# Kernel tuning notes

Hardware: AMD Instinct MI355X
Metric: run time of the kernel (lower is better)

The kernel has to match this reference:

```python
import jax, jax.numpy as jnp
import numpy as np

DECAY = 0.999
EPS = 1e-06
NUM_CLUSTERS = 512
NUM_HEADS = 8
DIM_PER_HEAD = 64


def setup_inputs() -> dict:
    key = jax.random.key(0)
    k1, k2 = jax.random.split(key)
    x = jax.random.normal(k1, (8, 2048, NUM_HEADS * DIM_PER_HEAD), dtype=jnp.float32)
    means = jax.random.normal(k2, (NUM_HEADS, NUM_CLUSTERS, DIM_PER_HEAD), dtype=jnp.float32)
    return {"x": x, "means": means}


def reference(x, means):
    b, n, _ = x.shape
    h, k, d = means.shape
    xh = x.reshape(b, n, h, d)  # 'b n (h d) -> b n h d'
    dists = (
        jnp.sum(xh ** 2, axis=-1)[..., None]
        - 2.0 * jnp.einsum('bnhd,hkd->bnhk', xh, means)
        + jnp.sum(means ** 2, axis=-1)[None, None, :, :]
    )
    cluster_ids = jnp.argmin(dists, axis=-1)  # [b, n, h] int
    # training-path EMA codebook update
    one_hot = jax.nn.one_hot(cluster_ids, k, dtype=jnp.float32)  # [b, n, h, k]
    per_cluster_count = jnp.sum(one_hot, axis=(0, 1))  # [h, k]
    sum_x = jnp.einsum('bnhk,bnhd->hkd', one_hot, xh)  # [h, k, d]
    new_means = sum_x / (EPS + per_cluster_count[..., None])
    updated_means = (1.0 - DECAY) * new_means + DECAY * means
    return cluster_ids, updated_means
```

## Files before the change

### kernel.cpp

```cpp
#include <hip/hip_runtime.h>

#define NUM_HEADS 8
#define DIM 64
#define NCLUST 512
#define NTOK 16384
#define ROWLEN 512
#define NIDS (NTOK * NUM_HEADS)
#define NMEANS (NUM_HEADS * NCLUST * DIM)
#define NCK (NUM_HEADS * NCLUST)
#define TPB 128
#define KQ 128
#define CAP 8
#define DELTA 0.35f

typedef unsigned long long u64;
typedef short bf16x8 __attribute__((ext_vector_type(8)));
typedef float f32x4 __attribute__((ext_vector_type(4)));

__device__ __forceinline__ unsigned short f2bf(float f) {
    unsigned b = __float_as_uint(f);
    return (unsigned short)((b + 0x7fffu + ((b >> 16) & 1u)) >> 16);
}
__device__ __forceinline__ unsigned pack2bf(float lo, float hi) {
    return (unsigned)f2bf(lo) | ((unsigned)f2bf(hi) << 16);
}
__device__ __forceinline__ float bf2f(unsigned short b) {
    return __uint_as_float((unsigned)b << 16);
}
__device__ __forceinline__ u64 packkey(float s, int k) {
    unsigned u = __float_as_uint(s);
    unsigned ord = (u & 0x80000000u) ? ~u : (u | 0x80000000u);
    return ((u64)(~ord) << 32) | (unsigned)k;
}
__device__ __forceinline__ int swz(int row, int byte_in_row) {
    return row * 128 + (byte_in_row ^ ((row & 7) << 4));
}

__global__ void vq_prep(const float* __restrict__ means,
                        float* __restrict__ q,
                        unsigned short* __restrict__ mbf) {
    int g = blockIdx.x * blockDim.x + threadIdx.x;
    int row = g >> 4, c = g & 15;
    float4 v = *(const float4*)(means + (size_t)row * DIM + c * 4);
    ushort4 b;
    b.x = f2bf(v.x); b.y = f2bf(v.y); b.z = f2bf(v.z); b.w = f2bf(v.w);
    *(ushort4*)(mbf + (size_t)row * DIM + c * 4) = b;
    float s = fmaf(v.x, v.x, fmaf(v.y, v.y, fmaf(v.z, v.z, v.w * v.w)));
#pragma unroll
    for (int off = 1; off < 16; off <<= 1) s += __shfl_xor(s, off, 64);
    if (c == 0) q[row] = 0.5f * s;
}

__global__ __launch_bounds__(256, 4) void vq_score(const float* __restrict__ x,
                                                   const float* __restrict__ means,
                                                   const unsigned short* __restrict__ mbf,
                                                   const float* __restrict__ q,
                                                   float* __restrict__ ids_f) {
    __shared__ __align__(16) unsigned char msq[KQ * 128];
    __shared__ __align__(16) unsigned char xbb[TPB * 128];
    __shared__ float qs[NCLUST];
    __shared__ int cnt[TPB];
    __shared__ unsigned short candL[TPB][CAP];

    const int head = blockIdx.y;
    const int t0   = blockIdx.x * TPB;
    const int tid  = threadIdx.x;
    const int wv = tid >> 6, l = tid & 63;
    const int lg = l >> 4, lc = l & 15;
    const int twave = wv * 32;

    uint4 pf0, pf1, pf2, pf3;
    auto loadq = [&](int qt) {
        int row = tid >> 1, c = tid & 1;
        const uint4* src = (const uint4*)(mbf +
            ((size_t)head * NCLUST + qt * KQ + row) * DIM + c * 32);
        pf0 = src[0]; pf1 = src[1]; pf2 = src[2]; pf3 = src[3];
    };
    auto writems = [&]() {
        int row = tid >> 1, c = tid & 1;
        *(uint4*)(msq + swz(row, c * 64 + 0))  = pf0;
        *(uint4*)(msq + swz(row, c * 64 + 16)) = pf1;
        *(uint4*)(msq + swz(row, c * 64 + 32)) = pf2;
        *(uint4*)(msq + swz(row, c * 64 + 48)) = pf3;
    };

#pragma unroll
    for (int it = 0; it < 2; ++it) {
        int tok = (tid >> 2) + it * 64;
        int c = tid & 3;
        const float4* src = (const float4*)(x + (size_t)(t0 + tok) * ROWLEN + head * DIM + c * 16);
        float4 v0 = src[0], v1 = src[1], v2 = src[2], v3 = src[3];
        uint4 lo, hi;
        lo.x = pack2bf(v0.x, v0.y); lo.y = pack2bf(v0.z, v0.w);
        lo.z = pack2bf(v1.x, v1.y); lo.w = pack2bf(v1.z, v1.w);
        hi.x = pack2bf(v2.x, v2.y); hi.y = pack2bf(v2.z, v2.w);
        hi.z = pack2bf(v3.x, v3.y); hi.w = pack2bf(v3.z, v3.w);
        *(uint4*)(xbb + swz(tok, c * 32 + 0))  = lo;
        *(uint4*)(xbb + swz(tok, c * 32 + 16)) = hi;
    }
    qs[tid] = q[head * NCLUST + tid];
    qs[tid + 256] = q[head * NCLUST + tid + 256];
    if (tid < TPB) cnt[tid] = 0;
    loadq(0);
    __syncthreads();

    bf16x8 af[2][2];
#pragma unroll
    for (int tt = 0; tt < 2; ++tt)
#pragma unroll
        for (int ks = 0; ks < 2; ++ks)
            af[tt][ks] = *(const bf16x8*)(xbb + swz(twave + tt * 16 + lc, ks * 64 + lg * 16));

    float best[2][4];
#pragma unroll
    for (int tt = 0; tt < 2; ++tt)
#pragma unroll
        for (int r = 0; r < 4; ++r) best[tt][r] = -3.0e38f;
    float thr[2][4];

    auto sweep1_q = [&](int qt) {
        const int rbase = 511 - qt * KQ - lc;
#pragma unroll
        for (int ct = 0; ct < KQ / 16; ++ct) {
            bf16x8 b0 = *(const bf16x8*)(msq + swz(ct * 16 + lc, 0 + lg * 16));
            bf16x8 b1 = *(const bf16x8*)(msq + swz(ct * 16 + lc, 64 + lg * 16));
            float qv = qs[qt * KQ + ct * 16 + lc];
            int rk = rbase - ct * 16;
#pragma unroll
            for (int tt = 0; tt < 2; ++tt) {
                f32x4 acc = (f32x4){-qv, -qv, -qv, -qv};
                acc = __builtin_amdgcn_mfma_f32_16x16x32_bf16(af[tt][0], b0, acc, 0, 0, 0);
                acc = __builtin_amdgcn_mfma_f32_16x16x32_bf16(af[tt][1], b1, acc, 0, 0, 0);
#pragma unroll
                for (int r = 0; r < 4; ++r) {
                    float v = __uint_as_float((__float_as_uint(acc[r]) & 0xFFFFFE00u) | (unsigned)rk);
                    best[tt][r] = fmaxf(best[tt][r], v);
                }
            }
        }
    };
    auto collect_q = [&](int qt) {
#pragma unroll
        for (int ct = 0; ct < KQ / 16; ++ct) {
            bf16x8 b0 = *(const bf16x8*)(msq + swz(ct * 16 + lc, 0 + lg * 16));
            bf16x8 b1 = *(const bf16x8*)(msq + swz(ct * 16 + lc, 64 + lg * 16));
            float qv = qs[qt * KQ + ct * 16 + lc];
            int k = qt * KQ + ct * 16 + lc;
#pragma unroll
            for (int tt = 0; tt < 2; ++tt) {
                f32x4 acc = (f32x4){-qv, -qv, -qv, -qv};
                acc = __builtin_amdgcn_mfma_f32_16x16x32_bf16(af[tt][0], b0, acc, 0, 0, 0);
                acc = __builtin_amdgcn_mfma_f32_16x16x32_bf16(af[tt][1], b1, acc, 0, 0, 0);
#pragma unroll
                for (int r = 0; r < 4; ++r) {
                    if (acc[r] >= thr[tt][r]) {
                        int tok = twave + tt * 16 + lg * 4 + r;
                        int slot = atomicAdd(&cnt[tok], 1);
                        if (slot < CAP) candL[tok][slot] = (unsigned short)k;
                    }
                }
            }
        }
    };

    for (int qt = 0; qt < 4; ++qt) {
        __syncthreads();
        writems();
        if (qt < 3) loadq(qt + 1);
        __syncthreads();
        sweep1_q(qt);
    }
#pragma unroll
    for (int tt = 0; tt < 2; ++tt)
#pragma unroll
        for (int r = 0; r < 4; ++r) {
#pragma unroll
            for (int off = 1; off < 16; off <<= 1)
                best[tt][r] = fmaxf(best[tt][r], __shfl_xor(best[tt][r], off, 64));
            thr[tt][r] = best[tt][r] - DELTA;
        }

    loadq(2);
    collect_q(3);
    for (int qt = 2; qt >= 0; --qt) {
        __syncthreads();
        writems();
        if (qt > 0) loadq(qt - 1);
        __syncthreads();
        collect_q(qt);
    }
    __syncthreads();

#pragma unroll 2
    for (int g = 0; g < 8; ++g) {
        int tok = twave + g * 4 + lg;
        int n = cnt[tok]; n = n < CAP ? n : CAP;
        const float4 xv = *(const float4*)(x + (size_t)(t0 + tok) * ROWLEN + head * DIM + lc * 4);
        u64 bk = ~0ull;
        for (int j = 0; j < n; ++j) {
            int k = candL[tok][j];
            const float4 mv = *(const float4*)(means + ((size_t)head * NCLUST + k) * DIM + lc * 4);
            float p = fmaf(xv.x, mv.x, fmaf(xv.y, mv.y, fmaf(xv.z, mv.z, xv.w * mv.w)));
#pragma unroll
            for (int off = 1; off < 16; off <<= 1) p += __shfl_xor(p, off, 64);
            u64 cd = packkey(p - qs[k], k);
            bk = cd < bk ? cd : bk;
        }
        if (lc == 0) ids_f[(size_t)(t0 + tok) * NUM_HEADS + head] = (float)(unsigned)(bk & 0x1ffu);
    }
}

__global__ void vq_scatter(const float* __restrict__ x,
                           const float* __restrict__ ids_f,
                           float* __restrict__ counts,
                           unsigned short* __restrict__ sums_bf,
                           int rep_mask) {
    int g = blockIdx.x * blockDim.x + threadIdx.x;
    int p = g >> 5;
    int l32 = threadIdx.x & 31;
    int token = p >> 3;
    int h = p & 7;
    int rep = token & rep_mask;
    int id = (int)ids_f[p];
    float2 xv = *(const float2*)(x + (size_t)token * ROWLEN + h * DIM + l32 * 2);
    unsigned val = pack2bf(xv.x, xv.y);
    unsigned short* dst = sums_bf + (size_t)rep * NMEANS
                        + (((size_t)h * NCLUST + id) << 6) + l32 * 2;
    asm volatile("global_atomic_pk_add_bf16 %0, %1, off" :: "v"(dst), "v"(val) : "memory");
    if (l32 == 0) atomicAdd(&counts[rep * NCK + h * NCLUST + id], 1.0f);
}

__global__ void vq_final(const float* __restrict__ means,
                         const float* __restrict__ counts,
                         const unsigned short* __restrict__ sums_bf,
                         float* __restrict__ out_means,
                         int nrep) {
    int i = blockIdx.x * blockDim.x + threadIdx.x;
    int ck = i >> 6;
    float c = 0.f, s = 0.f;
    for (int r = 0; r < nrep; ++r) {
        c += counts[r * NCK + ck];
        s += bf2f(sums_bf[(size_t)r * NMEANS + i]);
    }
    float nm = s / (1e-6f + c);
    out_means[i] = 0.999f * means[i] + 0.001f * nm;
}

extern "C" void kernel_launch(void* const* d_in, const int* in_sizes, int n_in,
                              void* d_out, int out_size, void* d_ws, size_t ws_size,
                              hipStream_t stream) {
    const float* x     = (const float*)d_in[0];
    const float* means = (const float*)d_in[1];

    float* out       = (float*)d_out;
    float* ids_f     = out;
    float* out_means = out + NIDS;

    float*          q   = (float*)d_ws;
    unsigned short* mbf = (unsigned short*)(q + NCK);
    float*          fbase = (float*)(mbf + NMEANS);
    size_t core = (size_t)((char*)fbase - (char*)d_ws);

    size_t per_rep = (size_t)NCK * sizeof(float) + (size_t)NMEANS * sizeof(unsigned short);
    int nrep = 1;
    for (int r = 8; r > 1; r >>= 1) {
        if (ws_size >= core + (size_t)r * per_rep) { nrep = r; break; }
    }
    float*          counts  = fbase;
    unsigned short* sums_bf = (unsigned short*)(counts + (size_t)nrep * NCK);

    hipMemsetAsync(counts, 0, (size_t)nrep * per_rep, stream);

    vq_prep<<<(NCK * 16) / 256, 256, 0, stream>>>(means, q, mbf);

    dim3 gs(NTOK / TPB, NUM_HEADS);
    vq_score<<<gs, 256, 0, stream>>>(x, means, mbf, q, ids_f);

    vq_scatter<<<(NIDS * 32) / 256, 256, 0, stream>>>(x, ids_f, counts, sums_bf, nrep - 1);

    vq_final<<<NMEANS / 256, 256, 0, stream>>>(means, counts, sums_bf, out_means, nrep);
}
```

Before: 78.14 us.

## Halve tokens per block, load x fragments directly into registers

Tokens per block drop from 128 to 64, so each wave handles 16 tokens instead of 32. The x staging buffer in shared memory is removed, and each lane now loads its MFMA A-fragment straight from global memory and converts it to bf16. Launch bounds rise to 8 blocks per CU to allow more occupancy thanks to fewer registers and less LDS. In exchange, the grid doubles, so the codebook tiles are streamed through shared memory twice as often per token, and there is less MFMA reuse per B-fragment load.

```diff
diff --git a/kernel.cpp b/kernel.cpp
--- a/kernel.cpp
+++ b/kernel.cpp
@@ -8,7 +8,7 @@
 #define NIDS (NTOK * NUM_HEADS)
 #define NMEANS (NUM_HEADS * NCLUST * DIM)
 #define NCK (NUM_HEADS * NCLUST)
-#define TPB 128
+#define TPB 64
 #define KQ 128
 #define CAP 8
 #define DELTA 0.35f
@@ -51,13 +51,12 @@
     if (c == 0) q[row] = 0.5f * s;
 }
 
-__global__ __launch_bounds__(256, 4) void vq_score(const float* __restrict__ x,
+__global__ __launch_bounds__(256, 8) void vq_score(const float* __restrict__ x,
                                                    const float* __restrict__ means,
                                                    const unsigned short* __restrict__ mbf,
                                                    const float* __restrict__ q,
                                                    float* __restrict__ ids_f) {
     __shared__ __align__(16) unsigned char msq[KQ * 128];
-    __shared__ __align__(16) unsigned char xbb[TPB * 128];
     __shared__ float qs[NCLUST];
     __shared__ int cnt[TPB];
     __shared__ unsigned short candL[TPB][CAP];
@@ -67,7 +66,7 @@
     const int tid  = threadIdx.x;
     const int wv = tid >> 6, l = tid & 63;
     const int lg = l >> 4, lc = l & 15;
-    const int twave = wv * 32;
+    const int twave = wv * 16;
 
     uint4 pf0, pf1, pf2, pf3;
     auto loadq = [&](int qt) {
@@ -84,39 +83,27 @@
         *(uint4*)(msq + swz(row, c * 64 + 48)) = pf3;
     };
 
-#pragma unroll
-    for (int it = 0; it < 2; ++it) {
-        int tok = (tid >> 2) + it * 64;
-        int c = tid & 3;
-        const float4* src = (const float4*)(x + (size_t)(t0 + tok) * ROWLEN + head * DIM + c * 16);
-        float4 v0 = src[0], v1 = src[1], v2 = src[2], v3 = src[3];
-        uint4 lo, hi;
-        lo.x = pack2bf(v0.x, v0.y); lo.y = pack2bf(v0.z, v0.w);
-        lo.z = pack2bf(v1.x, v1.y); lo.w = pack2bf(v1.z, v1.w);
-        hi.x = pack2bf(v2.x, v2.y); hi.y = pack2bf(v2.z, v2.w);
-        hi.z = pack2bf(v3.x, v3.y); hi.w = pack2bf(v3.z, v3.w);
-        *(uint4*)(xbb + swz(tok, c * 32 + 0))  = lo;
-        *(uint4*)(xbb + swz(tok, c * 32 + 16)) = hi;
+    bf16x8 af[2];
+    {
+        const float* xrow = x + (size_t)(t0 + twave + lc) * ROWLEN + head * DIM;
+#pragma unroll
+        for (int ks = 0; ks < 2; ++ks) {
+            float av[8];
+            *(float4*)&av[0] = *(const float4*)(xrow + ks * 32 + lg * 8);
+            *(float4*)&av[4] = *(const float4*)(xrow + ks * 32 + lg * 8 + 4);
+#pragma unroll
+            for (int j = 0; j < 8; ++j) af[ks][j] = (short)f2bf(av[j]);
+        }
     }
     qs[tid] = q[head * NCLUST + tid];
     qs[tid + 256] = q[head * NCLUST + tid + 256];
     if (tid < TPB) cnt[tid] = 0;
     loadq(0);
-    __syncthreads();
-
-    bf16x8 af[2][2];
-#pragma unroll
-    for (int tt = 0; tt < 2; ++tt)
-#pragma unroll
-        for (int ks = 0; ks < 2; ++ks)
-            af[tt][ks] = *(const bf16x8*)(xbb + swz(twave + tt * 16 + lc, ks * 64 + lg * 16));
-
-    float best[2][4];
-#pragma unroll
-    for (int tt = 0; tt < 2; ++tt)
-#pragma unroll
-        for (int r = 0; r < 4; ++r) best[tt][r] = -3.0e38f;
-    float thr[2][4];
+
+    float best[4];
+#pragma unroll
+    for (int r = 0; r < 4; ++r) best[r] = -3.0e38f;
+    float thr[4];
 
     auto sweep1_q = [&](int qt) {
         const int rbase = 511 - qt * KQ - lc;
@@ -126,16 +113,13 @@
             bf16x8 b1 = *(const bf16x8*)(msq + swz(ct * 16 + lc, 64 + lg * 16));
             float qv = qs[qt * KQ + ct * 16 + lc];
             int rk = rbase - ct * 16;
-#pragma unroll
-            for (int tt = 0; tt < 2; ++tt) {
-                f32x4 acc = (f32x4){-qv, -qv, -qv, -qv};
-                acc = __builtin_amdgcn_mfma_f32_16x16x32_bf16(af[tt][0], b0, acc, 0, 0, 0);
-                acc = __builtin_amdgcn_mfma_f32_16x16x32_bf16(af[tt][1], b1, acc, 0, 0, 0);
-#pragma unroll
-                for (int r = 0; r < 4; ++r) {
-                    float v = __uint_as_float((__float_as_uint(acc[r]) & 0xFFFFFE00u) | (unsigned)rk);
-                    best[tt][r] = fmaxf(best[tt][r], v);
-                }
+            f32x4 acc = (f32x4){-qv, -qv, -qv, -qv};
+            acc = __builtin_amdgcn_mfma_f32_16x16x32_bf16(af[0], b0, acc, 0, 0, 0);
+            acc = __builtin_amdgcn_mfma_f32_16x16x32_bf16(af[1], b1, acc, 0, 0, 0);
+#pragma unroll
+            for (int r = 0; r < 4; ++r) {
+                float v = __uint_as_float((__float_as_uint(acc[r]) & 0xFFFFFE00u) | (unsigned)rk);
+                best[r] = fmaxf(best[r], v);
             }
         }
     };
@@ -146,18 +130,15 @@
             bf16x8 b1 = *(const bf16x8*)(msq + swz(ct * 16 + lc, 64 + lg * 16));
             float qv = qs[qt * KQ + ct * 16 + lc];
             int k = qt * KQ + ct * 16 + lc;
-#pragma unroll
-            for (int tt = 0; tt < 2; ++tt) {
-                f32x4 acc = (f32x4){-qv, -qv, -qv, -qv};
-                acc = __builtin_amdgcn_mfma_f32_16x16x32_bf16(af[tt][0], b0, acc, 0, 0, 0);
-                acc = __builtin_amdgcn_mfma_f32_16x16x32_bf16(af[tt][1], b1, acc, 0, 0, 0);
-#pragma unroll
-                for (int r = 0; r < 4; ++r) {
-                    if (acc[r] >= thr[tt][r]) {
-                        int tok = twave + tt * 16 + lg * 4 + r;
-                        int slot = atomicAdd(&cnt[tok], 1);
-                        if (slot < CAP) candL[tok][slot] = (unsigned short)k;
-                    }
+            f32x4 acc = (f32x4){-qv, -qv, -qv, -qv};
+            acc = __builtin_amdgcn_mfma_f32_16x16x32_bf16(af[0], b0, acc, 0, 0, 0);
+            acc = __builtin_amdgcn_mfma_f32_16x16x32_bf16(af[1], b1, acc, 0, 0, 0);
+#pragma unroll
+            for (int r = 0; r < 4; ++r) {
+                if (acc[r] >= thr[r]) {
+                    int tok = twave + lg * 4 + r;
+                    int slot = atomicAdd(&cnt[tok], 1);
+                    if (slot < CAP) candL[tok][slot] = (unsigned short)k;
                 }
             }
         }
@@ -171,14 +152,12 @@
         sweep1_q(qt);
     }
 #pragma unroll
-    for (int tt = 0; tt < 2; ++tt)
-#pragma unroll
-        for (int r = 0; r < 4; ++r) {
-#pragma unroll
-            for (int off = 1; off < 16; off <<= 1)
-                best[tt][r] = fmaxf(best[tt][r], __shfl_xor(best[tt][r], off, 64));
-            thr[tt][r] = best[tt][r] - DELTA;
-        }
+    for (int r = 0; r < 4; ++r) {
+#pragma unroll
+        for (int off = 1; off < 16; off <<= 1)
+            best[r] = fmaxf(best[r], __shfl_xor(best[r], off, 64));
+        thr[r] = best[r] - DELTA;
+    }
 
     loadq(2);
     collect_q(3);
@@ -191,8 +170,8 @@
     }
     __syncthreads();
 
-#pragma unroll 2
-    for (int g = 0; g < 8; ++g) {
+#pragma unroll
+    for (int g = 0; g < 4; ++g) {
         int tok = twave + g * 4 + lg;
         int n = cnt[tok]; n = n < CAP ? n : CAP;
         const float4 xv = *(const float4*)(x + (size_t)(t0 + tok) * ROWLEN + head * DIM + lc * 4);
```

After: 96.17 us. 1.23x slower.
